# Kernel tuning notes

Measured on AMD Instinct MI355X. Metric: run time of the kernel, lower is better.

The kernel has to match this reference:

```python
import jax, jax.numpy as jnp
import numpy as np

NUM_HEADS = 32
NUM_KV_HEADS = 8
HEAD_DIM = 128
SCALE = 0.08838834764831845  # 1/sqrt(128)
NUM_SEQS = 8
Q_LEN = 256            # new tokens per sequence (uniform cu_seqlens_q)
MAX_PAGES = 128
PAGE_SIZE = 16
BLOCK_SIZE = 32
NUM_PAGES = NUM_SEQS * MAX_PAGES


def setup_inputs() -> dict:
    key = jax.random.key(0)
    ks = jax.random.split(key, 6)
    total = NUM_SEQS * Q_LEN
    q = jax.random.normal(ks[0], (total, NUM_HEADS * HEAD_DIM), dtype=jnp.float32)
    k = jax.random.normal(ks[1], (total, NUM_KV_HEADS * HEAD_DIM), dtype=jnp.float32)
    v = jax.random.normal(ks[2], (total, NUM_KV_HEADS * HEAD_DIM), dtype=jnp.float32)
    k_cache = jax.random.normal(ks[3], (NUM_PAGES, PAGE_SIZE, NUM_KV_HEADS, HEAD_DIM), dtype=jnp.float32)
    v_cache = jax.random.normal(ks[4], (NUM_PAGES, PAGE_SIZE, NUM_KV_HEADS, HEAD_DIM), dtype=jnp.float32)
    page_tables = jnp.arange(NUM_SEQS * MAX_PAGES, dtype=jnp.int32).reshape(NUM_SEQS, MAX_PAGES)
    context_lens = jax.random.randint(ks[5], (NUM_SEQS,), 0, MAX_PAGES * PAGE_SIZE, dtype=jnp.int32)
    return {
        'q': q, 'k': k, 'v': v,
        'k_cache': k_cache, 'v_cache': v_cache,
        'page_tables': page_tables, 'context_lens': context_lens,
        'page_size': PAGE_SIZE, 'block_size': BLOCK_SIZE,
    }


def reference(q, k, v, k_cache, v_cache, page_tables, context_lens, page_size, block_size):
    B, P = page_tables.shape
    S = q.shape[0] // B
    C = P * page_size                      # max cached context per seq
    G = NUM_HEADS // NUM_KV_HEADS          # GQA group size

    qb = q.reshape(B, S, NUM_KV_HEADS, G, HEAD_DIM)
    kb = k.reshape(B, S, NUM_KV_HEADS, HEAD_DIM)
    vb = v.reshape(B, S, NUM_KV_HEADS, HEAD_DIM)

    # page-table gather of cached K/V: [B, P, page_size, nkvh, hd] -> [B, C, nkvh, hd]
    k_ctx = k_cache[page_tables].reshape(B, C, NUM_KV_HEADS, HEAD_DIM)
    v_ctx = v_cache[page_tables].reshape(B, C, NUM_KV_HEADS, HEAD_DIM)

    k_full = jnp.concatenate([k_ctx, kb], axis=1)  # [B, C+S, nkvh, hd]
    v_full = jnp.concatenate([v_ctx, vb], axis=1)

    T = C + S
    t_idx = jnp.arange(T)
    s_idx = jnp.arange(S)
    # cached positions valid iff t < context_len; new positions use block mask
    ctx_valid = t_idx[None, :] < context_lens[:, None]            # [B, T]
    block_ends = (s_idx // block_size + 1) * block_size           # [S]
    new_valid = block_ends[:, None] > (t_idx[None, :] - C)        # [S, T]
    is_ctx = t_idx < C                                            # [T]
    mask = jnp.where(is_ctx[None, None, :], ctx_valid[:, None, :], new_valid[None, :, :])  # [B, S, T]

    # scores: [B, nkvh, G, S, T]
    scores = jnp.einsum('bsngd,btnd->bngst', qb, k_full) * SCALE
    scores = jnp.where(mask[:, None, None, :, :], scores, jnp.float32(-1e30))
    probs = jax.nn.softmax(scores, axis=-1)
    out = jnp.einsum('bngst,btnd->bsngd', probs, v_full)          # [B, S, nkvh, G, hd]
    return out.reshape(B * S, NUM_HEADS * HEAD_DIM)
```

## Files before the change

### kernel.cpp

```cpp
#include <hip/hip_runtime.h>
#include <hip/hip_bf16.h>

#define NUM_HEADS   32
#define NUM_KV_HEADS 8
#define HEAD_DIM    128
#define GQA          4
#define Q_LEN      256
#define MAX_PAGES  128
#define PAGE_SIZE   16
#define SCALE 0.08838834764831845f
#define LOG2E 1.44269504088896340736f
#define RESCALE_THR 8.0f

#define NCH_MAX   36
#define CHUNK_B   16384
#define KSTREAM   ((size_t)NCH_MAX * CHUNK_B)
#define NITEMS    512

typedef __bf16 bf16x8 __attribute__((ext_vector_type(8)));
typedef float  f32x4  __attribute__((ext_vector_type(4)));

union B8 { uint4 u; bf16x8 v; };

__device__ __forceinline__ unsigned f2bf(float x){
    unsigned u = __builtin_bit_cast(unsigned, x);
    return (u + 0x7fffu + ((u >> 16) & 1u)) >> 16;
}
__device__ __forceinline__ unsigned pack2(float lo, float hi){
    return f2bf(lo) | (f2bf(hi) << 16);
}

typedef __attribute__((address_space(3))) unsigned char lds_as3_t;
typedef const __attribute__((address_space(1))) void gas_v;
typedef __attribute__((address_space(3))) void las_v;

#define GLD16(g, l) __builtin_amdgcn_global_load_lds((gas_v*)(g), (las_v*)(l), 16, 0, 0)

#define TRR(dst, base, OFF) asm volatile("ds_read_b64_tr_b16 %0, %1 offset:" OFF \
                                         : "=v"(dst) : "v"(base))

__global__ __launch_bounds__(256) void prep_kernel(
    const float* __restrict__ knew,
    const float* __restrict__ vnew,
    const float* __restrict__ kcache,
    const float* __restrict__ vcache,
    const int*   __restrict__ ptab,
    const int*   __restrict__ ctxlens,
    unsigned char* __restrict__ kimg,
    unsigned char* __restrict__ vimg)
{
    const int ch  = blockIdx.x;
    const int kvh = blockIdx.y;
    const int b   = blockIdx.z;
    const int ctxlen = ctxlens[b];
    const int lim = ctxlen + Q_LEN;
    const int base = ch * 64;
    if (base >= lim) return;

    const int tid  = threadIdx.x;
    const int srow = tid >> 2;
    const int seg  = tid & 3;
    const int t    = base + srow;

    unsigned char* kdst = kimg + (size_t)(b * 8 + kvh) * KSTREAM + (size_t)ch * CHUNK_B;
    unsigned char* vdst = vimg + (size_t)(b * 8 + kvh) * KSTREAM + (size_t)ch * CHUNK_B;
    const int swz    = (srow & 7) << 4;
    const int vbyte0 = (srow >> 2) * 128 + (srow & 3) * 32;

    if (t < lim){
        size_t roff;
        const float *ksrc, *vsrc;
        if (t < ctxlen){
            const int page = ptab[b * MAX_PAGES + (t >> 4)];
            roff = ((size_t)(page * PAGE_SIZE + (t & 15)) * NUM_KV_HEADS + kvh) * HEAD_DIM;
            ksrc = kcache + roff; vsrc = vcache + roff;
        } else {
            roff = ((size_t)(b * Q_LEN + (t - ctxlen)) * NUM_KV_HEADS + kvh) * HEAD_DIM;
            ksrc = knew + roff; vsrc = vnew + roff;
        }
        const float* kr = ksrc + seg * 32;
        const float* vr = vsrc + seg * 32;
        #pragma unroll
        for (int i = 0; i < 4; ++i){
            float4 a  = *(const float4*)(kr + i * 8);
            float4 c4 = *(const float4*)(kr + i * 8 + 4);
            uint4 wv;
            wv.x = pack2(a.x, a.y);  wv.y = pack2(a.z, a.w);
            wv.z = pack2(c4.x, c4.y); wv.w = pack2(c4.z, c4.w);
            *(uint4*)(kdst + srow * 256 + ((seg * 64 + i * 16) ^ swz)) = wv;
        }
        #pragma unroll
        for (int db = 0; db < 2; ++db){
            const float4 a0 = *(const float4*)(vr + db * 16 + 0);
            const float4 a1 = *(const float4*)(vr + db * 16 + 4);
            const float4 a2 = *(const float4*)(vr + db * 16 + 8);
            const float4 a3 = *(const float4*)(vr + db * 16 + 12);
            uint4 w0, w1;
            w0.x = pack2(a0.x, a0.y); w0.y = pack2(a0.z, a0.w);
            w0.z = pack2(a1.x, a1.y); w0.w = pack2(a1.z, a1.w);
            w1.x = pack2(a2.x, a2.y); w1.y = pack2(a2.z, a2.w);
            w1.z = pack2(a3.x, a3.y); w1.w = pack2(a3.z, a3.w);
            const int dbk = seg * 2 + db;
            *(uint4*)(vdst + dbk * 2048 + vbyte0)      = w0;
            *(uint4*)(vdst + dbk * 2048 + vbyte0 + 16) = w1;
        }
    } else {
        const uint4 z = {0u, 0u, 0u, 0u};
        #pragma unroll
        for (int i = 0; i < 4; ++i)
            *(uint4*)(kdst + srow * 256 + ((seg * 64 + i * 16) ^ swz)) = z;
        #pragma unroll
        for (int db = 0; db < 2; ++db){
            const int dbk = seg * 2 + db;
            *(uint4*)(vdst + dbk * 2048 + vbyte0)      = z;
            *(uint4*)(vdst + dbk * 2048 + vbyte0 + 16) = z;
        }
    }
}

__global__ __launch_bounds__(256, 2) void attn_kernel(
    const float* __restrict__ q,
    const int*   __restrict__ ctxlens,
    float*       __restrict__ out,
    const unsigned char* __restrict__ kimg,
    const unsigned char* __restrict__ vimg,
    int* __restrict__ counter)
{
    __shared__ __align__(16) unsigned char lds[65536];
    int* s_item_p = (int*)(lds + 65532);

    const int tid  = threadIdx.x;
    const int w    = tid >> 6;
    const int lane = tid & 63;
    const int hh   = lane >> 4;
    const int cq   = lane & 15;

    const unsigned ldsb3 = (unsigned)(unsigned long long)(lds_as3_t*)(&lds[0]);

    for (;;){
        if (tid == 0) *s_item_p = atomicAdd(counter, 1);
        __syncthreads();
        const int it = *s_item_p;
        if (it >= NITEMS) return;

        const int b   = it & 7;
        const int kvh = (it >> 3) & 7;
        const int s32 = 7 - (it >> 6);

        const int s0 = s32 * 32;
        const int ctxlen = ctxlens[b];
        const int vlim = ctxlen + (s32 + 1) * 32;
        const int nch  = (vlim + 63) >> 6;
        const int hq   = kvh * GQA + w;

        const unsigned char* kstream = kimg + (size_t)(b * 8 + kvh) * KSTREAM;
        const unsigned char* vstream = vimg + (size_t)(b * 8 + kvh) * KSTREAM;

        #define STAGE(CH, PB) do { \
            const unsigned char* kg_ = kstream + (size_t)(CH) * CHUNK_B + (w * 4096 + lane * 16); \
            const unsigned char* vg_ = vstream + (size_t)(CH) * CHUNK_B + (w * 4096 + lane * 16); \
            _Pragma("unroll") \
            for (int i_ = 0; i_ < 4; ++i_){ \
                GLD16(kg_ + i_ * 1024, lds + (PB) * CHUNK_B + w * 4096 + i_ * 1024); \
                GLD16(vg_ + i_ * 1024, lds + 32768 + (PB) * CHUNK_B + w * 4096 + i_ * 1024); \
            } \
        } while (0)

        STAGE(0, 0);

        B8 qf[2][4];
        #pragma unroll
        for (int u = 0; u < 2; ++u){
            const float* qrow = q + (size_t)(b * Q_LEN + s0 + u * 16 + cq) * (NUM_HEADS * HEAD_DIM)
                                  + hq * HEAD_DIM;
            #pragma unroll
            for (int c = 0; c < 4; ++c){
                const float4 f0 = *(const float4*)(qrow + c * 32 + 8 * hh);
                const float4 f1 = *(const float4*)(qrow + c * 32 + 8 * hh + 4);
                const float sc = SCALE * LOG2E;
                qf[u][c].u.x = pack2(f0.x * sc, f0.y * sc);
                qf[u][c].u.y = pack2(f0.z * sc, f0.w * sc);
                qf[u][c].u.z = pack2(f1.x * sc, f1.y * sc);
                qf[u][c].u.w = pack2(f1.z * sc, f1.w * sc);
            }
        }

        f32x4 acc[2][8] = {};
        float mrun[2] = {-1e30f, -1e30f};
        float lp[2]   = {0.f, 0.f};

        __syncthreads();

        for (int ch = 0; ch < nch; ++ch){
            const int pb = ch & 1;
            if (ch + 1 < nch) STAGE(ch + 1, pb ^ 1);

            const int base = ch * 64;
            const unsigned kldsb = pb * CHUNK_B;

            __builtin_amdgcn_s_setprio(1);
            f32x4 st[2][4] = {};
            #pragma unroll
            for (int c = 0; c < 4; ++c){
                #pragma unroll
                for (int tf = 0; tf < 4; ++tf){
                    const int trow = tf * 16 + cq;
                    const unsigned byte = kldsb + trow * 256 + ((c * 64 + hh * 16) ^ ((trow & 7) << 4));
                    B8 kf; kf.u = *(const uint4*)(lds + byte);
                    st[0][tf] = __builtin_amdgcn_mfma_f32_16x16x32_bf16(kf.v, qf[0][c].v, st[0][tf], 0, 0, 0);
                    st[1][tf] = __builtin_amdgcn_mfma_f32_16x16x32_bf16(kf.v, qf[1][c].v, st[1][tf], 0, 0, 0);
                }
            }
            __builtin_amdgcn_s_setprio(0);

            B8 af[2][2];
            const bool interior = (base + 64 <= vlim);
            #pragma unroll
            for (int u = 0; u < 2; ++u){
                float p[4][4];
                float pm = -1e30f;
                if (interior){
                    #pragma unroll
                    for (int tf = 0; tf < 4; ++tf){
                        #pragma unroll
                        for (int r = 0; r < 4; ++r){
                            const float s = st[u][tf][r];
                            p[tf][r] = s;
                            pm = fmaxf(pm, s);
                        }
                    }
                } else {
                    #pragma unroll
                    for (int tf = 0; tf < 4; ++tf){
                        #pragma unroll
                        for (int r = 0; r < 4; ++r){
                            const int t = base + tf * 16 + hh * 4 + r;
                            const float s = (t < vlim) ? st[u][tf][r] : -1e30f;
                            p[tf][r] = s;
                            pm = fmaxf(pm, s);
                        }
                    }
                }
                pm = fmaxf(pm, __shfl_xor(pm, 16));
                pm = fmaxf(pm, __shfl_xor(pm, 32));

                if (!__all(pm <= mrun[u] + RESCALE_THR)){
                    const float mnew  = fmaxf(mrun[u], pm);
                    const float alpha = __builtin_amdgcn_exp2f(mrun[u] - mnew);
                    mrun[u] = mnew;
                    lp[u] *= alpha;
                    float a4[4];
                    #pragma unroll
                    for (int r = 0; r < 4; ++r) a4[r] = __shfl(alpha, hh * 20 + r);
                    #pragma unroll
                    for (int dc = 0; dc < 8; ++dc){
                        #pragma unroll
                        for (int r = 0; r < 4; ++r) acc[u][dc][r] *= a4[r];
                    }
                }
                const float m = mrun[u];
                float rsum = 0.f;
                #pragma unroll
                for (int tf = 0; tf < 4; ++tf){
                    #pragma unroll
                    for (int r = 0; r < 4; ++r){
                        const float e = __builtin_amdgcn_exp2f(p[tf][r] - m);
                        p[tf][r] = e;
                        rsum += e;
                    }
                }
                lp[u] += rsum;

                unsigned pk01[4], pk23[4];
                #pragma unroll
                for (int tf = 0; tf < 4; ++tf){
                    pk01[tf] = pack2(p[tf][0], p[tf][1]);
                    pk23[tf] = pack2(p[tf][2], p[tf][3]);
                }
                af[u][0].u.x = pk01[0]; af[u][0].u.y = pk23[0]; af[u][0].u.z = pk01[1]; af[u][0].u.w = pk23[1];
                af[u][1].u.x = pk01[2]; af[u][1].u.y = pk23[2]; af[u][1].u.z = pk01[3]; af[u][1].u.w = pk23[3];
            }

            {
                const unsigned trb = ldsb3 + 32768u + (unsigned)(pb * CHUNK_B) + (unsigned)(hh * 128 + cq * 8);
                unsigned long long r0,r1,r2,r3,r4,r5,r6,r7;
                B8 vf;
                __builtin_amdgcn_s_setprio(1);
                TRR(r0, trb, "0");     TRR(r1, trb, "512");
                TRR(r2, trb, "2048");  TRR(r3, trb, "2560");
                TRR(r4, trb, "4096");  TRR(r5, trb, "4608");
                TRR(r6, trb, "6144");  TRR(r7, trb, "6656");
                asm volatile("s_waitcnt lgkmcnt(0)" ::: "memory");
                __builtin_amdgcn_sched_barrier(0);
                vf.u.x=(unsigned)r0; vf.u.y=(unsigned)(r0>>32); vf.u.z=(unsigned)r1; vf.u.w=(unsigned)(r1>>32);
                acc[0][0] = __builtin_amdgcn_mfma_f32_16x16x32_bf16(af[0][0].v, vf.v, acc[0][0], 0, 0, 0);
                acc[1][0] = __builtin_amdgcn_mfma_f32_16x16x32_bf16(af[1][0].v, vf.v, acc[1][0], 0, 0, 0);
                vf.u.x=(unsigned)r2; vf.u.y=(unsigned)(r2>>32); vf.u.z=(unsigned)r3; vf.u.w=(unsigned)(r3>>32);
                acc[0][1] = __builtin_amdgcn_mfma_f32_16x16x32_bf16(af[0][0].v, vf.v, acc[0][1], 0, 0, 0);
                acc[1][1] = __builtin_amdgcn_mfma_f32_16x16x32_bf16(af[1][0].v, vf.v, acc[1][1], 0, 0, 0);
                vf.u.x=(unsigned)r4; vf.u.y=(unsigned)(r4>>32); vf.u.z=(unsigned)r5; vf.u.w=(unsigned)(r5>>32);
                acc[0][2] = __builtin_amdgcn_mfma_f32_16x16x32_bf16(af[0][0].v, vf.v, acc[0][2], 0, 0, 0);
                acc[1][2] = __builtin_amdgcn_mfma_f32_16x16x32_bf16(af[1][0].v, vf.v, acc[1][2], 0, 0, 0);
                vf.u.x=(unsigned)r6; vf.u.y=(unsigned)(r6>>32); vf.u.z=(unsigned)r7; vf.u.w=(unsigned)(r7>>32);
                acc[0][3] = __builtin_amdgcn_mfma_f32_16x16x32_bf16(af[0][0].v, vf.v, acc[0][3], 0, 0, 0);
                acc[1][3] = __builtin_amdgcn_mfma_f32_16x16x32_bf16(af[1][0].v, vf.v, acc[1][3], 0, 0, 0);
                TRR(r0, trb, "8192");  TRR(r1, trb, "8704");
                TRR(r2, trb, "10240"); TRR(r3, trb, "10752");
                TRR(r4, trb, "12288"); TRR(r5, trb, "12800");
                TRR(r6, trb, "14336"); TRR(r7, trb, "14848");
                asm volatile("s_waitcnt lgkmcnt(0)" ::: "memory");
                __builtin_amdgcn_sched_barrier(0);
                vf.u.x=(unsigned)r0; vf.u.y=(unsigned)(r0>>32); vf.u.z=(unsigned)r1; vf.u.w=(unsigned)(r1>>32);
                acc[0][4] = __builtin_amdgcn_mfma_f32_16x16x32_bf16(af[0][0].v, vf.v, acc[0][4], 0, 0, 0);
                acc[1][4] = __builtin_amdgcn_mfma_f32_16x16x32_bf16(af[1][0].v, vf.v, acc[1][4], 0, 0, 0);
                vf.u.x=(unsigned)r2; vf.u.y=(unsigned)(r2>>32); vf.u.z=(unsigned)r3; vf.u.w=(unsigned)(r3>>32);
                acc[0][5] = __builtin_amdgcn_mfma_f32_16x16x32_bf16(af[0][0].v, vf.v, acc[0][5], 0, 0, 0);
                acc[1][5] = __builtin_amdgcn_mfma_f32_16x16x32_bf16(af[1][0].v, vf.v, acc[1][5], 0, 0, 0);
                vf.u.x=(unsigned)r4; vf.u.y=(unsigned)(r4>>32); vf.u.z=(unsigned)r5; vf.u.w=(unsigned)(r5>>32);
                acc[0][6] = __builtin_amdgcn_mfma_f32_16x16x32_bf16(af[0][0].v, vf.v, acc[0][6], 0, 0, 0);
                acc[1][6] = __builtin_amdgcn_mfma_f32_16x16x32_bf16(af[1][0].v, vf.v, acc[1][6], 0, 0, 0);
                vf.u.x=(unsigned)r6; vf.u.y=(unsigned)(r6>>32); vf.u.z=(unsigned)r7; vf.u.w=(unsigned)(r7>>32);
                acc[0][7] = __builtin_amdgcn_mfma_f32_16x16x32_bf16(af[0][0].v, vf.v, acc[0][7], 0, 0, 0);
                acc[1][7] = __builtin_amdgcn_mfma_f32_16x16x32_bf16(af[1][0].v, vf.v, acc[1][7], 0, 0, 0);
                TRR(r0, trb, "1024");  TRR(r1, trb, "1536");
                TRR(r2, trb, "3072");  TRR(r3, trb, "3584");
                TRR(r4, trb, "5120");  TRR(r5, trb, "5632");
                TRR(r6, trb, "7168");  TRR(r7, trb, "7680");
                asm volatile("s_waitcnt lgkmcnt(0)" ::: "memory");
                __builtin_amdgcn_sched_barrier(0);
                vf.u.x=(unsigned)r0; vf.u.y=(unsigned)(r0>>32); vf.u.z=(unsigned)r1; vf.u.w=(unsigned)(r1>>32);
                acc[0][0] = __builtin_amdgcn_mfma_f32_16x16x32_bf16(af[0][1].v, vf.v, acc[0][0], 0, 0, 0);
                acc[1][0] = __builtin_amdgcn_mfma_f32_16x16x32_bf16(af[1][1].v, vf.v, acc[1][0], 0, 0, 0);
                vf.u.x=(unsigned)r2; vf.u.y=(unsigned)(r2>>32); vf.u.z=(unsigned)r3; vf.u.w=(unsigned)(r3>>32);
                acc[0][1] = __builtin_amdgcn_mfma_f32_16x16x32_bf16(af[0][1].v, vf.v, acc[0][1], 0, 0, 0);
                acc[1][1] = __builtin_amdgcn_mfma_f32_16x16x32_bf16(af[1][1].v, vf.v, acc[1][1], 0, 0, 0);
                vf.u.x=(unsigned)r4; vf.u.y=(unsigned)(r4>>32); vf.u.z=(unsigned)r5; vf.u.w=(unsigned)(r5>>32);
                acc[0][2] = __builtin_amdgcn_mfma_f32_16x16x32_bf16(af[0][1].v, vf.v, acc[0][2], 0, 0, 0);
                acc[1][2] = __builtin_amdgcn_mfma_f32_16x16x32_bf16(af[1][1].v, vf.v, acc[1][2], 0, 0, 0);
                vf.u.x=(unsigned)r6; vf.u.y=(unsigned)(r6>>32); vf.u.z=(unsigned)r7; vf.u.w=(unsigned)(r7>>32);
                acc[0][3] = __builtin_amdgcn_mfma_f32_16x16x32_bf16(af[0][1].v, vf.v, acc[0][3], 0, 0, 0);
                acc[1][3] = __builtin_amdgcn_mfma_f32_16x16x32_bf16(af[1][1].v, vf.v, acc[1][3], 0, 0, 0);
                TRR(r0, trb, "9216");  TRR(r1, trb, "9728");
                TRR(r2, trb, "11264"); TRR(r3, trb, "11776");
                TRR(r4, trb, "13312"); TRR(r5, trb, "13824");
                TRR(r6, trb, "15360"); TRR(r7, trb, "15872");
                asm volatile("s_waitcnt lgkmcnt(0)" ::: "memory");
                __builtin_amdgcn_sched_barrier(0);
                vf.u.x=(unsigned)r0; vf.u.y=(unsigned)(r0>>32); vf.u.z=(unsigned)r1; vf.u.w=(unsigned)(r1>>32);
                acc[0][4] = __builtin_amdgcn_mfma_f32_16x16x32_bf16(af[0][1].v, vf.v, acc[0][4], 0, 0, 0);
                acc[1][4] = __builtin_amdgcn_mfma_f32_16x16x32_bf16(af[1][1].v, vf.v, acc[1][4], 0, 0, 0);
                vf.u.x=(unsigned)r2; vf.u.y=(unsigned)(r2>>32); vf.u.z=(unsigned)r3; vf.u.w=(unsigned)(r3>>32);
                acc[0][5] = __builtin_amdgcn_mfma_f32_16x16x32_bf16(af[0][1].v, vf.v, acc[0][5], 0, 0, 0);
                acc[1][5] = __builtin_amdgcn_mfma_f32_16x16x32_bf16(af[1][1].v, vf.v, acc[1][5], 0, 0, 0);
                vf.u.x=(unsigned)r4; vf.u.y=(unsigned)(r4>>32); vf.u.z=(unsigned)r5; vf.u.w=(unsigned)(r5>>32);
                acc[0][6] = __builtin_amdgcn_mfma_f32_16x16x32_bf16(af[0][1].v, vf.v, acc[0][6], 0, 0, 0);
                acc[1][6] = __builtin_amdgcn_mfma_f32_16x16x32_bf16(af[1][1].v, vf.v, acc[1][6], 0, 0, 0);
                vf.u.x=(unsigned)r6; vf.u.y=(unsigned)(r6>>32); vf.u.z=(unsigned)r7; vf.u.w=(unsigned)(r7>>32);
                acc[0][7] = __builtin_amdgcn_mfma_f32_16x16x32_bf16(af[0][1].v, vf.v, acc[0][7], 0, 0, 0);
                acc[1][7] = __builtin_amdgcn_mfma_f32_16x16x32_bf16(af[1][1].v, vf.v, acc[1][7], 0, 0, 0);
                __builtin_amdgcn_s_setprio(0);
            }
            __syncthreads();
        }

        #pragma unroll
        for (int u = 0; u < 2; ++u){
            float l = lp[u];
            l += __shfl_xor(l, 16);
            l += __shfl_xor(l, 32);
            const float li = 1.0f / l;
            float li4[4];
            #pragma unroll
            for (int r = 0; r < 4; ++r) li4[r] = __shfl(li, hh * 20 + r);
            #pragma unroll
            for (int dc = 0; dc < 8; ++dc){
                #pragma unroll
                for (int r = 0; r < 4; ++r){
                    const int so = s0 + u * 16 + hh * 4 + r;
                    out[(size_t)(b * Q_LEN + so) * (NUM_HEADS * HEAD_DIM) + hq * HEAD_DIM + dc * 16 + cq]
                        = acc[u][dc][r] * li4[r];
                }
            }
        }
        #undef STAGE
    }
}

#define VSTRIDE 2080

__global__ __launch_bounds__(256, 2) void pattn_fallback(
    const float* __restrict__ q,
    const float* __restrict__ knew,
    const float* __restrict__ vnew,
    const float* __restrict__ kcache,
    const float* __restrict__ vcache,
    const int*   __restrict__ ptab,
    const int*   __restrict__ ctxlens,
    float*       __restrict__ out)
{
    __shared__ unsigned short klds[64 * 128];
    __shared__ unsigned char  vlds[8 * VSTRIDE];

    const int s32   = blockIdx.x;
    const int kvh   = blockIdx.y;
    const int b     = blockIdx.z;
    const int tid   = threadIdx.x;
    const int w     = tid >> 6;
    const int lane  = tid & 63;
    const int hh    = lane >> 4;
    const int cq    = lane & 15;

    const int s0  = s32 * 32;
    const int NV  = (s32 + 1) * 32;
    const int ctxlen = ctxlens[b];
    const int nc1 = (ctxlen + 63) >> 6;
    const int nc2 = (NV + 63) >> 6;
    const int nch = nc1 + nc2;
    const int hq = kvh * GQA + w;

    const unsigned trbase =
        (unsigned)(unsigned long long)(lds_as3_t*)(&vlds[0]) + (unsigned)(hh * 128 + cq * 8);

    B8 qf[2][4];
    #pragma unroll
    for (int u = 0; u < 2; ++u){
        const float* qrow = q + (size_t)(b * Q_LEN + s0 + u * 16 + cq) * (NUM_HEADS * HEAD_DIM)
                              + hq * HEAD_DIM;
        #pragma unroll
        for (int c = 0; c < 4; ++c){
            const float4 f0 = *(const float4*)(qrow + c * 32 + 8 * hh);
            const float4 f1 = *(const float4*)(qrow + c * 32 + 8 * hh + 4);
            qf[u][c].u.x = pack2(f0.x * SCALE, f0.y * SCALE);
            qf[u][c].u.y = pack2(f0.z * SCALE, f0.w * SCALE);
            qf[u][c].u.z = pack2(f1.x * SCALE, f1.y * SCALE);
            qf[u][c].u.w = pack2(f1.z * SCALE, f1.w * SCALE);
        }
    }

    f32x4 acc[2][8] = {};
    float mrun[2] = {-1e30f, -1e30f};
    float lrun[2] = {0.f, 0.f};

    const int srow = tid >> 2;
    const int seg  = tid & 3;

    for (int ch = 0; ch < nch; ++ch){
        const bool cachedc = (ch < nc1);
        const int  base = cachedc ? ch * 64 : (ch - nc1) * 64;
        const int  vlim = cachedc ? ctxlen : NV;
        {
            const int t = base + srow;
            size_t roff;
            if (cachedc){
                const int page = ptab[b * MAX_PAGES + (t >> 4)];
                roff = ((size_t)(page * PAGE_SIZE + (t & 15)) * NUM_KV_HEADS + kvh) * HEAD_DIM;
            } else {
                roff = ((size_t)(b * Q_LEN + t) * NUM_KV_HEADS + kvh) * HEAD_DIM;
            }
            const float* kr = (cachedc ? kcache : knew) + roff + seg * 32;
            const float* vr = (cachedc ? vcache : vnew) + roff + seg * 32;
            const int swz = (srow & 7) << 4;
            #pragma unroll
            for (int i = 0; i < 4; ++i){
                float4 a  = *(const float4*)(kr + i * 8);
                float4 c4 = *(const float4*)(kr + i * 8 + 4);
                uint4 wv;
                wv.x = pack2(a.x, a.y);  wv.y = pack2(a.z, a.w);
                wv.z = pack2(c4.x, c4.y); wv.w = pack2(c4.z, c4.w);
                const int byte = srow * 256 + ((seg * 64 + i * 16) ^ swz);
                *(uint4*)((char*)klds + byte) = wv;
            }
            const int vbyte0 = (srow >> 2) * 128 + (srow & 3) * 32;
            #pragma unroll
            for (int db = 0; db < 2; ++db){
                const float4 a0 = *(const float4*)(vr + db * 16 + 0);
                const float4 a1 = *(const float4*)(vr + db * 16 + 4);
                const float4 a2 = *(const float4*)(vr + db * 16 + 8);
                const float4 a3 = *(const float4*)(vr + db * 16 + 12);
                uint4 w0, w1;
                w0.x = pack2(a0.x, a0.y); w0.y = pack2(a0.z, a0.w);
                w0.z = pack2(a1.x, a1.y); w0.w = pack2(a1.z, a1.w);
                w1.x = pack2(a2.x, a2.y); w1.y = pack2(a2.z, a2.w);
                w1.z = pack2(a3.x, a3.y); w1.w = pack2(a3.z, a3.w);
                const int dbk = seg * 2 + db;
                const int byte = dbk * VSTRIDE + vbyte0;
                *(uint4*)((char*)vlds + byte)      = w0;
                *(uint4*)((char*)vlds + byte + 16) = w1;
            }
        }
        __syncthreads();

        f32x4 st[2][4] = {};
        #pragma unroll
        for (int c = 0; c < 4; ++c){
            #pragma unroll
            for (int tf = 0; tf < 4; ++tf){
                const int trow = tf * 16 + cq;
                const int byte = trow * 256 + ((c * 64 + hh * 16) ^ ((trow & 7) << 4));
                B8 kf; kf.u = *(const uint4*)((const char*)klds + byte);
                st[0][tf] = __builtin_amdgcn_mfma_f32_16x16x32_bf16(kf.v, qf[0][c].v, st[0][tf], 0, 0, 0);
                st[1][tf] = __builtin_amdgcn_mfma_f32_16x16x32_bf16(kf.v, qf[1][c].v, st[1][tf], 0, 0, 0);
            }
        }

        B8 af[2][2];
        #pragma unroll
        for (int u = 0; u < 2; ++u){
            float p[4][4];
            float pm = -1e30f;
            #pragma unroll
            for (int tf = 0; tf < 4; ++tf){
                #pragma unroll
                for (int r = 0; r < 4; ++r){
                    const int t = base + tf * 16 + hh * 4 + r;
                    const float s = (t < vlim) ? st[u][tf][r] : -1e30f;
                    p[tf][r] = s;
                    pm = fmaxf(pm, s);
                }
            }
            pm = fmaxf(pm, __shfl_xor(pm, 16));
            pm = fmaxf(pm, __shfl_xor(pm, 32));
            const float mnew  = fmaxf(mrun[u], pm);
            const float alpha = __expf(mrun[u] - mnew);
            mrun[u] = mnew;
            float rsum = 0.f;
            #pragma unroll
            for (int tf = 0; tf < 4; ++tf){
                #pragma unroll
                for (int r = 0; r < 4; ++r){
                    const float e = __expf(p[tf][r] - mnew);
                    p[tf][r] = e;
                    rsum += e;
                }
            }
            rsum += __shfl_xor(rsum, 16);
            rsum += __shfl_xor(rsum, 32);
            lrun[u] = lrun[u] * alpha + rsum;

            float a4[4];
            #pragma unroll
            for (int r = 0; r < 4; ++r) a4[r] = __shfl(alpha, hh * 20 + r);
            #pragma unroll
            for (int dc = 0; dc < 8; ++dc){
                #pragma unroll
                for (int r = 0; r < 4; ++r) acc[u][dc][r] *= a4[r];
            }

            unsigned pk01[4], pk23[4];
            #pragma unroll
            for (int tf = 0; tf < 4; ++tf){
                pk01[tf] = pack2(p[tf][0], p[tf][1]);
                pk23[tf] = pack2(p[tf][2], p[tf][3]);
            }
            af[u][0].u.x = pk01[0]; af[u][0].u.y = pk23[0]; af[u][0].u.z = pk01[1]; af[u][0].u.w = pk23[1];
            af[u][1].u.x = pk01[2]; af[u][1].u.y = pk23[2]; af[u][1].u.z = pk01[3]; af[u][1].u.w = pk23[3];
        }

        {
            unsigned long long r0,r1,r2,r3,r4,r5,r6,r7;
            B8 vf;
            TRR(r0, trbase, "0");     TRR(r1, trbase, "512");
            TRR(r2, trbase, "2080");  TRR(r3, trbase, "2592");
            TRR(r4, trbase, "4160");  TRR(r5, trbase, "4672");
            TRR(r6, trbase, "6240");  TRR(r7, trbase, "6752");
            asm volatile("s_waitcnt lgkmcnt(0)" ::: "memory");
            __builtin_amdgcn_sched_barrier(0);
            vf.u.x=(unsigned)r0; vf.u.y=(unsigned)(r0>>32); vf.u.z=(unsigned)r1; vf.u.w=(unsigned)(r1>>32);
            acc[0][0] = __builtin_amdgcn_mfma_f32_16x16x32_bf16(af[0][0].v, vf.v, acc[0][0], 0, 0, 0);
            acc[1][0] = __builtin_amdgcn_mfma_f32_16x16x32_bf16(af[1][0].v, vf.v, acc[1][0], 0, 0, 0);
            vf.u.x=(unsigned)r2; vf.u.y=(unsigned)(r2>>32); vf.u.z=(unsigned)r3; vf.u.w=(unsigned)(r3>>32);
            acc[0][1] = __builtin_amdgcn_mfma_f32_16x16x32_bf16(af[0][0].v, vf.v, acc[0][1], 0, 0, 0);
            acc[1][1] = __builtin_amdgcn_mfma_f32_16x16x32_bf16(af[1][0].v, vf.v, acc[1][1], 0, 0, 0);
            vf.u.x=(unsigned)r4; vf.u.y=(unsigned)(r4>>32); vf.u.z=(unsigned)r5; vf.u.w=(unsigned)(r5>>32);
            acc[0][2] = __builtin_amdgcn_mfma_f32_16x16x32_bf16(af[0][0].v, vf.v, acc[0][2], 0, 0, 0);
            acc[1][2] = __builtin_amdgcn_mfma_f32_16x16x32_bf16(af[1][0].v, vf.v, acc[1][2], 0, 0, 0);
            vf.u.x=(unsigned)r6; vf.u.y=(unsigned)(r6>>32); vf.u.z=(unsigned)r7; vf.u.w=(unsigned)(r7>>32);
            acc[0][3] = __builtin_amdgcn_mfma_f32_16x16x32_bf16(af[0][0].v, vf.v, acc[0][3], 0, 0, 0);
            acc[1][3] = __builtin_amdgcn_mfma_f32_16x16x32_bf16(af[1][0].v, vf.v, acc[1][3], 0, 0, 0);
            TRR(r0, trbase, "8320");  TRR(r1, trbase, "8832");
            TRR(r2, trbase, "10400"); TRR(r3, trbase, "10912");
            TRR(r4, trbase, "12480"); TRR(r5, trbase, "12992");
            TRR(r6, trbase, "14560"); TRR(r7, trbase, "15072");
            asm volatile("s_waitcnt lgkmcnt(0)" ::: "memory");
            __builtin_amdgcn_sched_barrier(0);
            vf.u.x=(unsigned)r0; vf.u.y=(unsigned)(r0>>32); vf.u.z=(unsigned)r1; vf.u.w=(unsigned)(r1>>32);
            acc[0][4] = __builtin_amdgcn_mfma_f32_16x16x32_bf16(af[0][0].v, vf.v, acc[0][4], 0, 0, 0);
            acc[1][4] = __builtin_amdgcn_mfma_f32_16x16x32_bf16(af[1][0].v, vf.v, acc[1][4], 0, 0, 0);
            vf.u.x=(unsigned)r2; vf.u.y=(unsigned)(r2>>32); vf.u.z=(unsigned)r3; vf.u.w=(unsigned)(r3>>32);
            acc[0][5] = __builtin_amdgcn_mfma_f32_16x16x32_bf16(af[0][0].v, vf.v, acc[0][5], 0, 0, 0);
            acc[1][5] = __builtin_amdgcn_mfma_f32_16x16x32_bf16(af[1][0].v, vf.v, acc[1][5], 0, 0, 0);
            vf.u.x=(unsigned)r4; vf.u.y=(unsigned)(r4>>32); vf.u.z=(unsigned)r5; vf.u.w=(unsigned)(r5>>32);
            acc[0][6] = __builtin_amdgcn_mfma_f32_16x16x32_bf16(af[0][0].v, vf.v, acc[0][6], 0, 0, 0);
            acc[1][6] = __builtin_amdgcn_mfma_f32_16x16x32_bf16(af[1][0].v, vf.v, acc[1][6], 0, 0, 0);
            vf.u.x=(unsigned)r6; vf.u.y=(unsigned)(r6>>32); vf.u.z=(unsigned)r7; vf.u.w=(unsigned)(r7>>32);
            acc[0][7] = __builtin_amdgcn_mfma_f32_16x16x32_bf16(af[0][0].v, vf.v, acc[0][7], 0, 0, 0);
            acc[1][7] = __builtin_amdgcn_mfma_f32_16x16x32_bf16(af[1][0].v, vf.v, acc[1][7], 0, 0, 0);
            TRR(r0, trbase, "1024");  TRR(r1, trbase, "1536");
            TRR(r2, trbase, "3104");  TRR(r3, trbase, "3616");
            TRR(r4, trbase, "5184");  TRR(r5, trbase, "5696");
            TRR(r6, trbase, "7264");  TRR(r7, trbase, "7776");
            asm volatile("s_waitcnt lgkmcnt(0)" ::: "memory");
            __builtin_amdgcn_sched_barrier(0);
            vf.u.x=(unsigned)r0; vf.u.y=(unsigned)(r0>>32); vf.u.z=(unsigned)r1; vf.u.w=(unsigned)(r1>>32);
            acc[0][0] = __builtin_amdgcn_mfma_f32_16x16x32_bf16(af[0][1].v, vf.v, acc[0][0], 0, 0, 0);
            acc[1][0] = __builtin_amdgcn_mfma_f32_16x16x32_bf16(af[1][1].v, vf.v, acc[1][0], 0, 0, 0);
            vf.u.x=(unsigned)r2; vf.u.y=(unsigned)(r2>>32); vf.u.z=(unsigned)r3; vf.u.w=(unsigned)(r3>>32);
            acc[0][1] = __builtin_amdgcn_mfma_f32_16x16x32_bf16(af[0][1].v, vf.v, acc[0][1], 0, 0, 0);
            acc[1][1] = __builtin_amdgcn_mfma_f32_16x16x32_bf16(af[1][1].v, vf.v, acc[1][1], 0, 0, 0);
            vf.u.x=(unsigned)r4; vf.u.y=(unsigned)(r4>>32); vf.u.z=(unsigned)r5; vf.u.w=(unsigned)(r5>>32);
            acc[0][2] = __builtin_amdgcn_mfma_f32_16x16x32_bf16(af[0][1].v, vf.v, acc[0][2], 0, 0, 0);
            acc[1][2] = __builtin_amdgcn_mfma_f32_16x16x32_bf16(af[1][1].v, vf.v, acc[1][2], 0, 0, 0);
            vf.u.x=(unsigned)r6; vf.u.y=(unsigned)(r6>>32); vf.u.z=(unsigned)r7; vf.u.w=(unsigned)(r7>>32);
            acc[0][3] = __builtin_amdgcn_mfma_f32_16x16x32_bf16(af[0][1].v, vf.v, acc[0][3], 0, 0, 0);
            acc[1][3] = __builtin_amdgcn_mfma_f32_16x16x32_bf16(af[1][1].v, vf.v, acc[1][3], 0, 0, 0);
            TRR(r0, trbase, "9344");  TRR(r1, trbase, "9856");
            TRR(r2, trbase, "11424"); TRR(r3, trbase, "11936");
            TRR(r4, trbase, "13504"); TRR(r5, trbase, "14016");
            TRR(r6, trbase, "15584"); TRR(r7, trbase, "16096");
            asm volatile("s_waitcnt lgkmcnt(0)" ::: "memory");
            __builtin_amdgcn_sched_barrier(0);
            vf.u.x=(unsigned)r0; vf.u.y=(unsigned)(r0>>32); vf.u.z=(unsigned)r1; vf.u.w=(unsigned)(r1>>32);
            acc[0][4] = __builtin_amdgcn_mfma_f32_16x16x32_bf16(af[0][1].v, vf.v, acc[0][4], 0, 0, 0);
            acc[1][4] = __builtin_amdgcn_mfma_f32_16x16x32_bf16(af[1][1].v, vf.v, acc[1][4], 0, 0, 0);
            vf.u.x=(unsigned)r2; vf.u.y=(unsigned)(r2>>32); vf.u.z=(unsigned)r3; vf.u.w=(unsigned)(r3>>32);
            acc[0][5] = __builtin_amdgcn_mfma_f32_16x16x32_bf16(af[0][1].v, vf.v, acc[0][5], 0, 0, 0);
            acc[1][5] = __builtin_amdgcn_mfma_f32_16x16x32_bf16(af[1][1].v, vf.v, acc[1][5], 0, 0, 0);
            vf.u.x=(unsigned)r4; vf.u.y=(unsigned)(r4>>32); vf.u.z=(unsigned)r5; vf.u.w=(unsigned)(r5>>32);
            acc[0][6] = __builtin_amdgcn_mfma_f32_16x16x32_bf16(af[0][1].v, vf.v, acc[0][6], 0, 0, 0);
            acc[1][6] = __builtin_amdgcn_mfma_f32_16x16x32_bf16(af[1][1].v, vf.v, acc[1][6], 0, 0, 0);
            vf.u.x=(unsigned)r6; vf.u.y=(unsigned)(r6>>32); vf.u.z=(unsigned)r7; vf.u.w=(unsigned)(r7>>32);
            acc[0][7] = __builtin_amdgcn_mfma_f32_16x16x32_bf16(af[0][1].v, vf.v, acc[0][7], 0, 0, 0);
            acc[1][7] = __builtin_amdgcn_mfma_f32_16x16x32_bf16(af[1][1].v, vf.v, acc[1][7], 0, 0, 0);
        }
        __syncthreads();
    }

    #pragma unroll
    for (int u = 0; u < 2; ++u){
        const float li = 1.0f / lrun[u];
        float li4[4];
        #pragma unroll
        for (int r = 0; r < 4; ++r) li4[r] = __shfl(li, hh * 20 + r);
        #pragma unroll
        for (int dc = 0; dc < 8; ++dc){
            #pragma unroll
            for (int r = 0; r < 4; ++r){
                const int so = s0 + u * 16 + hh * 4 + r;
                out[(size_t)(b * Q_LEN + so) * (NUM_HEADS * HEAD_DIM) + hq * HEAD_DIM + dc * 16 + cq]
                    = acc[u][dc][r] * li4[r];
            }
        }
    }
}

extern "C" void kernel_launch(void* const* d_in, const int* in_sizes, int n_in,
                              void* d_out, int out_size, void* d_ws, size_t ws_size,
                              hipStream_t stream) {
    const float* q  = (const float*)d_in[0];
    const float* k  = (const float*)d_in[1];
    const float* v  = (const float*)d_in[2];
    const float* kc = (const float*)d_in[3];
    const float* vc = (const float*)d_in[4];
    const int*   pt = (const int*)d_in[5];
    const int*   cl = (const int*)d_in[6];
    float* o = (float*)d_out;

    const size_t img_bytes = (size_t)64 * KSTREAM;
    const size_t need = 256 + 2 * img_bytes;

    if (ws_size >= need) {
        unsigned char* kimg = (unsigned char*)d_ws + 256;
        unsigned char* vimg = kimg + img_bytes;
        hipMemsetAsync(d_ws, 0, 4, stream);
        prep_kernel<<<dim3(NCH_MAX, 8, 8), 256, 0, stream>>>(k, v, kc, vc, pt, cl, kimg, vimg);
        attn_kernel<<<NITEMS, 256, 0, stream>>>(q, cl, o, kimg, vimg, (int*)d_ws);
    } else {
        dim3 grid(8, 8, 8);
        pattn_fallback<<<grid, 256, 0, stream>>>(q, k, v, kc, vc, pt, cl, o);
    }
}
```

Baseline: 134.2 us.

## Halve KV chunk size and deepen LDS pipeline to four stages

Shrinks each K/V chunk from 64 to 32 tokens, rewrites the prep kernel's image layout to match, and replaces the double buffer with a 4-slot ring holding three chunks in flight. Each iteration waits on vmcnt and issues one barrier instead of two __syncthreads. The goal is to hide global-to-LDS latency better and waste less work on partial final chunks, at the cost of more loop iterations and more per-chunk softmax and barrier overhead.

```diff
diff --git a/kernel.cpp b/kernel.cpp
--- a/kernel.cpp
+++ b/kernel.cpp
@@ -12,8 +12,8 @@
 #define LOG2E 1.44269504088896340736f
 #define RESCALE_THR 8.0f
 
-#define NCH_MAX   36
-#define CHUNK_B   16384
+#define NCH_MAX   72
+#define CHUNK_B   8192
 #define KSTREAM   ((size_t)NCH_MAX * CHUNK_B)
 #define NITEMS    512
 
@@ -54,18 +54,18 @@
     const int b   = blockIdx.z;
     const int ctxlen = ctxlens[b];
     const int lim = ctxlen + Q_LEN;
-    const int base = ch * 64;
+    const int base = ch * 32;
     if (base >= lim) return;
 
     const int tid  = threadIdx.x;
-    const int srow = tid >> 2;
-    const int seg  = tid & 3;
+    const int srow = tid >> 3;
+    const int seg  = tid & 7;
     const int t    = base + srow;
 
     unsigned char* kdst = kimg + (size_t)(b * 8 + kvh) * KSTREAM + (size_t)ch * CHUNK_B;
     unsigned char* vdst = vimg + (size_t)(b * 8 + kvh) * KSTREAM + (size_t)ch * CHUNK_B;
     const int swz    = (srow & 7) << 4;
-    const int vbyte0 = (srow >> 2) * 128 + (srow & 3) * 32;
+    const int vbyte0 = seg * 1024 + (srow >> 2) * 128 + (srow & 3) * 32;
 
     if (t < lim){
         size_t roff;
@@ -78,43 +78,37 @@
             roff = ((size_t)(b * Q_LEN + (t - ctxlen)) * NUM_KV_HEADS + kvh) * HEAD_DIM;
             ksrc = knew + roff; vsrc = vnew + roff;
         }
-        const float* kr = ksrc + seg * 32;
-        const float* vr = vsrc + seg * 32;
-        #pragma unroll
-        for (int i = 0; i < 4; ++i){
+        const float* kr = ksrc + seg * 16;
+        const float* vr = vsrc + seg * 16;
+        #pragma unroll
+        for (int i = 0; i < 2; ++i){
             float4 a  = *(const float4*)(kr + i * 8);
             float4 c4 = *(const float4*)(kr + i * 8 + 4);
             uint4 wv;
             wv.x = pack2(a.x, a.y);  wv.y = pack2(a.z, a.w);
             wv.z = pack2(c4.x, c4.y); wv.w = pack2(c4.z, c4.w);
-            *(uint4*)(kdst + srow * 256 + ((seg * 64 + i * 16) ^ swz)) = wv;
-        }
-        #pragma unroll
-        for (int db = 0; db < 2; ++db){
-            const float4 a0 = *(const float4*)(vr + db * 16 + 0);
-            const float4 a1 = *(const float4*)(vr + db * 16 + 4);
-            const float4 a2 = *(const float4*)(vr + db * 16 + 8);
-            const float4 a3 = *(const float4*)(vr + db * 16 + 12);
+            *(uint4*)(kdst + srow * 256 + ((seg * 32 + i * 16) ^ swz)) = wv;
+        }
+        {
+            const float4 a0 = *(const float4*)(vr + 0);
+            const float4 a1 = *(const float4*)(vr + 4);
+            const float4 a2 = *(const float4*)(vr + 8);
+            const float4 a3 = *(const float4*)(vr + 12);
             uint4 w0, w1;
             w0.x = pack2(a0.x, a0.y); w0.y = pack2(a0.z, a0.w);
             w0.z = pack2(a1.x, a1.y); w0.w = pack2(a1.z, a1.w);
             w1.x = pack2(a2.x, a2.y); w1.y = pack2(a2.z, a2.w);
             w1.z = pack2(a3.x, a3.y); w1.w = pack2(a3.z, a3.w);
-            const int dbk = seg * 2 + db;
-            *(uint4*)(vdst + dbk * 2048 + vbyte0)      = w0;
-            *(uint4*)(vdst + dbk * 2048 + vbyte0 + 16) = w1;
+            *(uint4*)(vdst + vbyte0)      = w0;
+            *(uint4*)(vdst + vbyte0 + 16) = w1;
         }
     } else {
         const uint4 z = {0u, 0u, 0u, 0u};
         #pragma unroll
-        for (int i = 0; i < 4; ++i)
-            *(uint4*)(kdst + srow * 256 + ((seg * 64 + i * 16) ^ swz)) = z;
-        #pragma unroll
-        for (int db = 0; db < 2; ++db){
-            const int dbk = seg * 2 + db;
-            *(uint4*)(vdst + dbk * 2048 + vbyte0)      = z;
-            *(uint4*)(vdst + dbk * 2048 + vbyte0 + 16) = z;
-        }
+        for (int i = 0; i < 2; ++i)
+            *(uint4*)(kdst + srow * 256 + ((seg * 32 + i * 16) ^ swz)) = z;
+        *(uint4*)(vdst + vbyte0)      = z;
+        *(uint4*)(vdst + vbyte0 + 16) = z;
     }
 }
 
@@ -150,20 +144,19 @@
         const int s0 = s32 * 32;
         const int ctxlen = ctxlens[b];
         const int vlim = ctxlen + (s32 + 1) * 32;
-        const int nch  = (vlim + 63) >> 6;
+        const int nch  = (vlim + 31) >> 5;
         const int hq   = kvh * GQA + w;
 
         const unsigned char* kstream = kimg + (size_t)(b * 8 + kvh) * KSTREAM;
         const unsigned char* vstream = vimg + (size_t)(b * 8 + kvh) * KSTREAM;
 
-        #define STAGE(CH, PB) do { \
-            const unsigned char* kg_ = kstream + (size_t)(CH) * CHUNK_B + (w * 4096 + lane * 16); \
-            const unsigned char* vg_ = vstream + (size_t)(CH) * CHUNK_B + (w * 4096 + lane * 16); \
-            _Pragma("unroll") \
-            for (int i_ = 0; i_ < 4; ++i_){ \
-                GLD16(kg_ + i_ * 1024, lds + (PB) * CHUNK_B + w * 4096 + i_ * 1024); \
-                GLD16(vg_ + i_ * 1024, lds + 32768 + (PB) * CHUNK_B + w * 4096 + i_ * 1024); \
-            } \
+        #define STAGE(CH, BI) do { \
+            const unsigned char* kg_ = kstream + (size_t)(CH) * CHUNK_B + (w * 1024 + lane * 16); \
+            const unsigned char* vg_ = vstream + (size_t)(CH) * CHUNK_B + (w * 1024 + lane * 16); \
+            GLD16(kg_,        lds + (BI) * 8192 + w * 1024); \
+            GLD16(kg_ + 4096, lds + (BI) * 8192 + w * 1024 + 4096); \
+            GLD16(vg_,        lds + 32768 + (BI) * 8192 + w * 1024); \
+            GLD16(vg_ + 4096, lds + 32768 + (BI) * 8192 + w * 1024 + 4096); \
         } while (0)
 
         STAGE(0, 0);
@@ -185,27 +178,35 @@
             }
         }
 
+        if (1 < nch) STAGE(1, 1);
+        if (2 < nch) STAGE(2, 2);
+
         f32x4 acc[2][8] = {};
         float mrun[2] = {-1e30f, -1e30f};
         float lp[2]   = {0.f, 0.f};
 
-        __syncthreads();
-
         for (int ch = 0; ch < nch; ++ch){
-            const int pb = ch & 1;
-            if (ch + 1 < nch) STAGE(ch + 1, pb ^ 1);
-
-            const int base = ch * 64;
-            const unsigned kldsb = pb * CHUNK_B;
+            const int rem = nch - 1 - ch;
+            if (rem >= 2)      { asm volatile("s_waitcnt vmcnt(8)" ::: "memory"); }
+            else if (rem == 1) { asm volatile("s_waitcnt vmcnt(4)" ::: "memory"); }
+            else               { asm volatile("s_waitcnt vmcnt(0)" ::: "memory"); }
+            __builtin_amdgcn_sched_barrier(0);
+            __builtin_amdgcn_s_barrier();
+            __builtin_amdgcn_sched_barrier(0);
+
+            if (ch + 3 < nch) STAGE(ch + 3, (ch + 3) & 3);
+
+            const int base = ch * 32;
+            const unsigned kb = (unsigned)((ch & 3) * 8192);
 
             __builtin_amdgcn_s_setprio(1);
-            f32x4 st[2][4] = {};
+            f32x4 st[2][2] = {};
             #pragma unroll
             for (int c = 0; c < 4; ++c){
                 #pragma unroll
-                for (int tf = 0; tf < 4; ++tf){
+                for (int tf = 0; tf < 2; ++tf){
                     const int trow = tf * 16 + cq;
-                    const unsigned byte = kldsb + trow * 256 + ((c * 64 + hh * 16) ^ ((trow & 7) << 4));
+                    const unsigned byte = kb + trow * 256 + ((c * 64 + hh * 16) ^ ((trow & 7) << 4));
                     B8 kf; kf.u = *(const uint4*)(lds + byte);
                     st[0][tf] = __builtin_amdgcn_mfma_f32_16x16x32_bf16(kf.v, qf[0][c].v, st[0][tf], 0, 0, 0);
                     st[1][tf] = __builtin_amdgcn_mfma_f32_16x16x32_bf16(kf.v, qf[1][c].v, st[1][tf], 0, 0, 0);
@@ -213,15 +214,15 @@
             }
             __builtin_amdgcn_s_setprio(0);
 
-            B8 af[2][2];
-            const bool interior = (base + 64 <= vlim);
+            B8 af[2];
+            const bool interior = (base + 32 <= vlim);
             #pragma unroll
             for (int u = 0; u < 2; ++u){
-                float p[4][4];
+                float p[2][4];
                 float pm = -1e30f;
                 if (interior){
                     #pragma unroll
-                    for (int tf = 0; tf < 4; ++tf){
+                    for (int tf = 0; tf < 2; ++tf){
                         #pragma unroll
                         for (int r = 0; r < 4; ++r){
                             const float s = st[u][tf][r];
@@ -231,7 +232,7 @@
                     }
                 } else {
                     #pragma unroll
-                    for (int tf = 0; tf < 4; ++tf){
+                    for (int tf = 0; tf < 2; ++tf){
                         #pragma unroll
                         for (int r = 0; r < 4; ++r){
                             const int t = base + tf * 16 + hh * 4 + r;
@@ -261,7 +262,7 @@
                 const float m = mrun[u];
                 float rsum = 0.f;
                 #pragma unroll
-                for (int tf = 0; tf < 4; ++tf){
+                for (int tf = 0; tf < 2; ++tf){
                     #pragma unroll
                     for (int r = 0; r < 4; ++r){
                         const float e = __builtin_amdgcn_exp2f(p[tf][r] - m);
@@ -271,96 +272,56 @@
                 }
                 lp[u] += rsum;
 
-                unsigned pk01[4], pk23[4];
-                #pragma unroll
-                for (int tf = 0; tf < 4; ++tf){
-                    pk01[tf] = pack2(p[tf][0], p[tf][1]);
-                    pk23[tf] = pack2(p[tf][2], p[tf][3]);
-                }
-                af[u][0].u.x = pk01[0]; af[u][0].u.y = pk23[0]; af[u][0].u.z = pk01[1]; af[u][0].u.w = pk23[1];
-                af[u][1].u.x = pk01[2]; af[u][1].u.y = pk23[2]; af[u][1].u.z = pk01[3]; af[u][1].u.w = pk23[3];
+                af[u].u.x = pack2(p[0][0], p[0][1]);
+                af[u].u.y = pack2(p[0][2], p[0][3]);
+                af[u].u.z = pack2(p[1][0], p[1][1]);
+                af[u].u.w = pack2(p[1][2], p[1][3]);
             }
 
             {
-                const unsigned trb = ldsb3 + 32768u + (unsigned)(pb * CHUNK_B) + (unsigned)(hh * 128 + cq * 8);
+                const unsigned trb = ldsb3 + 32768u + (unsigned)((ch & 3) * 8192)
+                                   + (unsigned)(hh * 128 + cq * 8);
                 unsigned long long r0,r1,r2,r3,r4,r5,r6,r7;
                 B8 vf;
                 __builtin_amdgcn_s_setprio(1);
                 TRR(r0, trb, "0");     TRR(r1, trb, "512");
-                TRR(r2, trb, "2048");  TRR(r3, trb, "2560");
-                TRR(r4, trb, "4096");  TRR(r5, trb, "4608");
-                TRR(r6, trb, "6144");  TRR(r7, trb, "6656");
+                TRR(r2, trb, "1024");  TRR(r3, trb, "1536");
+                TRR(r4, trb, "2048");  TRR(r5, trb, "2560");
+                TRR(r6, trb, "3072");  TRR(r7, trb, "3584");
                 asm volatile("s_waitcnt lgkmcnt(0)" ::: "memory");
                 __builtin_amdgcn_sched_barrier(0);
                 vf.u.x=(unsigned)r0; vf.u.y=(unsigned)(r0>>32); vf.u.z=(unsigned)r1; vf.u.w=(unsigned)(r1>>32);
-                acc[0][0] = __builtin_amdgcn_mfma_f32_16x16x32_bf16(af[0][0].v, vf.v, acc[0][0], 0, 0, 0);
-                acc[1][0] = __builtin_amdgcn_mfma_f32_16x16x32_bf16(af[1][0].v, vf.v, acc[1][0], 0, 0, 0);
+                acc[0][0] = __builtin_amdgcn_mfma_f32_16x16x32_bf16(af[0].v, vf.v, acc[0][0], 0, 0, 0);
+                acc[1][0] = __builtin_amdgcn_mfma_f32_16x16x32_bf16(af[1].v, vf.v, acc[1][0], 0, 0, 0);
                 vf.u.x=(unsigned)r2; vf.u.y=(unsigned)(r2>>32); vf.u.z=(unsigned)r3; vf.u.w=(unsigned)(r3>>32);
-                acc[0][1] = __builtin_amdgcn_mfma_f32_16x16x32_bf16(af[0][0].v, vf.v, acc[0][1], 0, 0, 0);
-                acc[1][1] = __builtin_amdgcn_mfma_f32_16x16x32_bf16(af[1][0].v, vf.v, acc[1][1], 0, 0, 0);
+                acc[0][1] = __builtin_amdgcn_mfma_f32_16x16x32_bf16(af[0].v, vf.v, acc[0][1], 0, 0, 0);
+                acc[1][1] = __builtin_amdgcn_mfma_f32_16x16x32_bf16(af[1].v, vf.v, acc[1][1], 0, 0, 0);
                 vf.u.x=(unsigned)r4; vf.u.y=(unsigned)(r4>>32); vf.u.z=(unsigned)r5; vf.u.w=(unsigned)(r5>>32);
-                acc[0][2] = __builtin_amdgcn_mfma_f32_16x16x32_bf16(af[0][0].v, vf.v, acc[0][2], 0, 0, 0);
-                acc[1][2] = __builtin_amdgcn_mfma_f32_16x16x32_bf16(af[1][0].v, vf.v, acc[1][2], 0, 0, 0);
+                acc[0][2] = __builtin_amdgcn_mfma_f32_16x16x32_bf16(af[0].v, vf.v, acc[0][2], 0, 0, 0);
+                acc[1][2] = __builtin_amdgcn_mfma_f32_16x16x32_bf16(af[1].v, vf.v, acc[1][2], 0, 0, 0);
                 vf.u.x=(unsigned)r6; vf.u.y=(unsigned)(r6>>32); vf.u.z=(unsigned)r7; vf.u.w=(unsigned)(r7>>32);
-                acc[0][3] = __builtin_amdgcn_mfma_f32_16x16x32_bf16(af[0][0].v, vf.v, acc[0][3], 0, 0, 0);
-                acc[1][3] = __builtin_amdgcn_mfma_f32_16x16x32_bf16(af[1][0].v, vf.v, acc[1][3], 0, 0, 0);
-                TRR(r0, trb, "8192");  TRR(r1, trb, "8704");
-                TRR(r2, trb, "10240"); TRR(r3, trb, "10752");
-                TRR(r4, trb, "12288"); TRR(r5, trb, "12800");
-                TRR(r6, trb, "14336"); TRR(r7, trb, "14848");
-                asm volatile("s_waitcnt lgkmcnt(0)" ::: "memory");
-                __builtin_amdgcn_sched_barrier(0);
-                vf.u.x=(unsigned)r0; vf.u.y=(unsigned)(r0>>32); vf.u.z=(unsigned)r1; vf.u.w=(unsigned)(r1>>32);
-                acc[0][4] = __builtin_amdgcn_mfma_f32_16x16x32_bf16(af[0][0].v, vf.v, acc[0][4], 0, 0, 0);
-                acc[1][4] = __builtin_amdgcn_mfma_f32_16x16x32_bf16(af[1][0].v, vf.v, acc[1][4], 0, 0, 0);
-                vf.u.x=(unsigned)r2; vf.u.y=(unsigned)(r2>>32); vf.u.z=(unsigned)r3; vf.u.w=(unsigned)(r3>>32);
-                acc[0][5] = __builtin_amdgcn_mfma_f32_16x16x32_bf16(af[0][0].v, vf.v, acc[0][5], 0, 0, 0);
-                acc[1][5] = __builtin_amdgcn_mfma_f32_16x16x32_bf16(af[1][0].v, vf.v, acc[1][5], 0, 0, 0);
-                vf.u.x=(unsigned)r4; vf.u.y=(unsigned)(r4>>32); vf.u.z=(unsigned)r5; vf.u.w=(unsigned)(r5>>32);
-                acc[0][6] = __builtin_amdgcn_mfma_f32_16x16x32_bf16(af[0][0].v, vf.v, acc[0][6], 0, 0, 0);
-                acc[1][6] = __builtin_amdgcn_mfma_f32_16x16x32_bf16(af[1][0].v, vf.v, acc[1][6], 0, 0, 0);
-                vf.u.x=(unsigned)r6; vf.u.y=(unsigned)(r6>>32); vf.u.z=(unsigned)r7; vf.u.w=(unsigned)(r7>>32);
-                acc[0][7] = __builtin_amdgcn_mfma_f32_16x16x32_bf16(af[0][0].v, vf.v, acc[0][7], 0, 0, 0);
-                acc[1][7] = __builtin_amdgcn_mfma_f32_16x16x32_bf16(af[1][0].v, vf.v, acc[1][7], 0, 0, 0);
-                TRR(r0, trb, "1024");  TRR(r1, trb, "1536");
-                TRR(r2, trb, "3072");  TRR(r3, trb, "3584");
-                TRR(r4, trb, "5120");  TRR(r5, trb, "5632");
+                acc[0][3] = __builtin_amdgcn_mfma_f32_16x16x32_bf16(af[0].v, vf.v, acc[0][3], 0, 0, 0);
+                acc[1][3] = __builtin_amdgcn_mfma_f32_16x16x32_bf16(af[1].v, vf.v, acc[1][3], 0, 0, 0);
+                TRR(r0, trb, "4096");  TRR(r1, trb, "4608");
+                TRR(r2, trb, "5120");  TRR(r3, trb, "5632");
+                TRR(r4, trb, "6144");  TRR(r5, trb, "6656");
                 TRR(r6, trb, "7168");  TRR(r7, trb, "7680");
                 asm volatile("s_waitcnt lgkmcnt(0)" ::: "memory");
                 __builtin_amdgcn_sched_barrier(0);
                 vf.u.x=(unsigned)r0; vf.u.y=(unsigned)(r0>>32); vf.u.z=(unsigned)r1; vf.u.w=(unsigned)(r1>>32);
-                acc[0][0] = __builtin_amdgcn_mfma_f32_16x16x32_bf16(af[0][1].v, vf.v, acc[0][0], 0, 0, 0);
-                acc[1][0] = __builtin_amdgcn_mfma_f32_16x16x32_bf16(af[1][1].v, vf.v, acc[1][0], 0, 0, 0);
+                acc[0][4] = __builtin_amdgcn_mfma_f32_16x16x32_bf16(af[0].v, vf.v, acc[0][4], 0, 0, 0);
+                acc[1][4] = __builtin_amdgcn_mfma_f32_16x16x32_bf16(af[1].v, vf.v, acc[1][4], 0, 0, 0);
                 vf.u.x=(unsigned)r2; vf.u.y=(unsigned)(r2>>32); vf.u.z=(unsigned)r3; vf.u.w=(unsigned)(r3>>32);
-                acc[0][1] = __builtin_amdgcn_mfma_f32_16x16x32_bf16(af[0][1].v, vf.v, acc[0][1], 0, 0, 0);
-                acc[1][1] = __builtin_amdgcn_mfma_f32_16x16x32_bf16(af[1][1].v, vf.v, acc[1][1], 0, 0, 0);
+                acc[0][5] = __builtin_amdgcn_mfma_f32_16x16x32_bf16(af[0].v, vf.v, acc[0][5], 0, 0, 0);
+                acc[1][5] = __builtin_amdgcn_mfma_f32_16x16x32_bf16(af[1].v, vf.v, acc[1][5], 0, 0, 0);
                 vf.u.x=(unsigned)r4; vf.u.y=(unsigned)(r4>>32); vf.u.z=(unsigned)r5; vf.u.w=(unsigned)(r5>>32);
-                acc[0][2] = __builtin_amdgcn_mfma_f32_16x16x32_bf16(af[0][1].v, vf.v, acc[0][2], 0, 0, 0);
-                acc[1][2] = __builtin_amdgcn_mfma_f32_16x16x32_bf16(af[1][1].v, vf.v, acc[1][2], 0, 0, 0);
+                acc[0][6] = __builtin_amdgcn_mfma_f32_16x16x32_bf16(af[0].v, vf.v, acc[0][6], 0, 0, 0);
+                acc[1][6] = __builtin_amdgcn_mfma_f32_16x16x32_bf16(af[1].v, vf.v, acc[1][6], 0, 0, 0);
                 vf.u.x=(unsigned)r6; vf.u.y=(unsigned)(r6>>32); vf.u.z=(unsigned)r7; vf.u.w=(unsigned)(r7>>32);
-                acc[0][3] = __builtin_amdgcn_mfma_f32_16x16x32_bf16(af[0][1].v, vf.v, acc[0][3], 0, 0, 0);
-                acc[1][3] = __builtin_amdgcn_mfma_f32_16x16x32_bf16(af[1][1].v, vf.v, acc[1][3], 0, 0, 0);
-                TRR(r0, trb, "9216");  TRR(r1, trb, "9728");
-                TRR(r2, trb, "11264"); TRR(r3, trb, "11776");
-                TRR(r4, trb, "13312"); TRR(r5, trb, "13824");
-                TRR(r6, trb, "15360"); TRR(r7, trb, "15872");
-                asm volatile("s_waitcnt lgkmcnt(0)" ::: "memory");
-                __builtin_amdgcn_sched_barrier(0);
-                vf.u.x=(unsigned)r0; vf.u.y=(unsigned)(r0>>32); vf.u.z=(unsigned)r1; vf.u.w=(unsigned)(r1>>32);
-                acc[0][4] = __builtin_amdgcn_mfma_f32_16x16x32_bf16(af[0][1].v, vf.v, acc[0][4], 0, 0, 0);
-                acc[1][4] = __builtin_amdgcn_mfma_f32_16x16x32_bf16(af[1][1].v, vf.v, acc[1][4], 0, 0, 0);
-                vf.u.x=(unsigned)r2; vf.u.y=(unsigned)(r2>>32); vf.u.z=(unsigned)r3; vf.u.w=(unsigned)(r3>>32);
-                acc[0][5] = __builtin_amdgcn_mfma_f32_16x16x32_bf16(af[0][1].v, vf.v, acc[0][5], 0, 0, 0);
-                acc[1][5] = __builtin_amdgcn_mfma_f32_16x16x32_bf16(af[1][1].v, vf.v, acc[1][5], 0, 0, 0);
-                vf.u.x=(unsigned)r4; vf.u.y=(unsigned)(r4>>32); vf.u.z=(unsigned)r5; vf.u.w=(unsigned)(r5>>32);
-                acc[0][6] = __builtin_amdgcn_mfma_f32_16x16x32_bf16(af[0][1].v, vf.v, acc[0][6], 0, 0, 0);
-                acc[1][6] = __builtin_amdgcn_mfma_f32_16x16x32_bf16(af[1][1].v, vf.v, acc[1][6], 0, 0, 0);
-                vf.u.x=(unsigned)r6; vf.u.y=(unsigned)(r6>>32); vf.u.z=(unsigned)r7; vf.u.w=(unsigned)(r7>>32);
-                acc[0][7] = __builtin_amdgcn_mfma_f32_16x16x32_bf16(af[0][1].v, vf.v, acc[0][7], 0, 0, 0);
-                acc[1][7] = __builtin_amdgcn_mfma_f32_16x16x32_bf16(af[1][1].v, vf.v, acc[1][7], 0, 0, 0);
+                acc[0][7] = __builtin_amdgcn_mfma_f32_16x16x32_bf16(af[0].v, vf.v, acc[0][7], 0, 0, 0);
+                acc[1][7] = __builtin_amdgcn_mfma_f32_16x16x32_bf16(af[1].v, vf.v, acc[1][7], 0, 0, 0);
                 __builtin_amdgcn_s_setprio(0);
             }
-            __syncthreads();
         }
 
         #pragma unroll
```

New measurement: 139.9 us. 4.3% more time.
